# Kernel optimization log

Hardware: AMD Instinct MI355X
Metric: run time of the kernel (lower is better)

The kernel has to match this reference:

```python
import jax, jax.numpy as jnp
import numpy as np

# ---- cfg constants (JDE / YOLOv4-tracking style) ----
STRIDES = (8.0, 16.0, 32.0)
TRAIN_SIZE = 608.0
LEVELS = 3
NUM_ANCHORS = 4
EMB_DIM = 208
CONF_THRESH = 0.5
NMS_IOU = 0.45
K_LEVEL = 300   # proposals kept per level after confidence filtering
MAX_PROP = 500  # final padded proposal count per image
_ANCHORS = np.array([
    [[8, 24], [11, 34], [16, 48], [23, 68]],
    [[32, 96], [45, 135], [64, 192], [90, 271]],
    [[128, 384], [180, 540], [256, 640], [512, 640]],
], dtype=np.float32)  # [LEVELS, NUM_ANCHORS, 2] in pixels


def _decode_level(pred, emb, anchors_px, stride):
    """pred [B,A,H,W,6], emb [B,H,W,E] -> [B, A*H*W, 4+1+E] (xyxy in [0,1], conf, l2-norm emb)."""
    B, A, H, W, _ = pred.shape
    conf = jax.nn.softmax(pred[..., 4:6], axis=-1)[..., 1:2]  # [B,A,H,W,1]
    anc = anchors_px / stride  # anchors in grid units, [A,2]
    gy, gx = jnp.meshgrid(jnp.arange(H, dtype=pred.dtype),
                          jnp.arange(W, dtype=pred.dtype), indexing="ij")
    aw = anc[:, 0][:, None, None]  # [A,1,1]
    ah = anc[:, 1][:, None, None]
    # JDE-style delta decode: offsets scaled by anchor size, exp size decode
    x = pred[..., 0] * aw + gx
    y = pred[..., 1] * ah + gy
    w = jnp.exp(pred[..., 2]) * aw
    h = jnp.exp(pred[..., 3]) * ah
    scale = stride / TRAIN_SIZE  # back to pixels, then normalize by train size
    x1 = jnp.clip((x - 0.5 * w) * scale, 0.0, 1.0)
    y1 = jnp.clip((y - 0.5 * h) * scale, 0.0, 1.0)
    x2 = jnp.clip((x + 0.5 * w) * scale, 0.0, 1.0)
    y2 = jnp.clip((y + 0.5 * h) * scale, 0.0, 1.0)
    box = jnp.stack([x1, y1, x2, y2], axis=-1)  # [B,A,H,W,4]
    # tile embedding over anchors and l2-normalize (tf.math.l2_normalize, eps on sum of squares)
    pe = jnp.broadcast_to(emb[:, None], (B, A, H, W, emb.shape[-1]))
    n2 = jnp.sum(pe * pe, axis=-1, keepdims=True)
    pe = pe * jax.lax.rsqrt(jnp.maximum(n2, 1e-12))
    preds = jnp.concatenate([box, conf, pe], axis=-1)  # [B,A,H,W,4+1+E]
    return preds.reshape(B, A * H * W, preds.shape[-1])


def _conf_topk(props):
    """Confidence threshold + keep top K_LEVEL per image (zero-padded). props [B,N,D]."""
    s = props[..., 4]
    sm = jnp.where(s > CONF_THRESH, s, 0.0)
    top_s, top_i = jax.lax.top_k(sm, K_LEVEL)
    g = jnp.take_along_axis(props, top_i[..., None], axis=1)  # [B,K,D]
    return g * (top_s > 0.0)[..., None].astype(props.dtype)


def _nms_one(props):
    """Greedy NMS for one image. props [N,D] -> [MAX_PROP,D] zero-padded."""
    sc_in = props[:, 4]
    order = jnp.argsort(-sc_in)
    p = props[order]                      # sorted by score desc
    b, sc = p[:, :4], p[:, 4]
    N = b.shape[0]
    area = (b[:, 2] - b[:, 0]) * (b[:, 3] - b[:, 1])
    ix1 = jnp.maximum(b[:, None, 0], b[None, :, 0])
    iy1 = jnp.maximum(b[:, None, 1], b[None, :, 1])
    ix2 = jnp.minimum(b[:, None, 2], b[None, :, 2])
    iy2 = jnp.minimum(b[:, None, 3], b[None, :, 3])
    inter = jnp.clip(ix2 - ix1, 0.0) * jnp.clip(iy2 - iy1, 0.0)
    iou = inter / (area[:, None] + area[None, :] - inter + 1e-9)  # [N,N]
    idxs = jnp.arange(N)
    keep0 = sc > 0.0
    def step(keep, i):
        row = jnp.take(iou, i, axis=0)
        ki = jnp.take(keep, i)
        sup = ki & (row > NMS_IOU) & (idxs > i)
        return keep & jnp.logical_not(sup), None
    keep, _ = jax.lax.scan(step, keep0, idxs)
    keep = keep & (sc > 0.0)
    rank = jnp.cumsum(keep) - 1
    dest = jnp.where(keep & (rank < MAX_PROP), rank, MAX_PROP)  # out-of-range -> dropped
    out = jnp.zeros((MAX_PROP, p.shape[1]), p.dtype).at[dest].set(p, mode="drop")
    return out


def _forward(pred0, pred1, pred2, emb0, emb1, emb2):
    preds = (pred0, pred1, pred2)
    embs = (emb0, emb1, emb2)
    levels = []
    for i in range(LEVELS):
        pr = _decode_level(preds[i], embs[i], jnp.asarray(_ANCHORS[i]), STRIDES[i])
        levels.append(_conf_topk(pr))
    props = jnp.concatenate(levels, axis=1)        # [B, 3*K_LEVEL, 4+1+E]
    out = jax.vmap(_nms_one)(props)                # [B, MAX_PROP, 4+1+E]
    # entry_stop_gradients: grads only through non-zero (valid) entries
    mask = (jnp.sum(out[..., :4], axis=-1) != 0.0).astype(out.dtype)[..., None]
    return out * mask + jax.lax.stop_gradient(out) * (1.0 - mask)


def setup_inputs() -> dict:
    key = jax.random.key(0)
    ks = jax.random.split(key, 6)
    B = 16
    sizes = [76, 38, 19]  # TRAIN_SIZE // stride
    d = {}
    for i, hw in enumerate(sizes):
        d[f"pred{i}"] = jax.random.normal(ks[i], (B, NUM_ANCHORS, hw, hw, 6), jnp.float32)
        d[f"emb{i}"] = jax.random.normal(ks[3 + i], (B, hw, hw, EMB_DIM), jnp.float32)
    return d


def reference(pred0, pred1, pred2, emb0, emb1, emb2):
    return _forward(pred0, pred1, pred2, emb0, emb1, emb2)
```

## Files before the change

kernel.cpp:

```cpp
#include <hip/hip_runtime.h>

typedef unsigned long long u64;
typedef unsigned int u32;

#define KLVL 300
#define NPROP 900
#define MAXPROP 500
#define DDIM 213
#define EDIM 208

__constant__ float c_anc[3][4][2] = {
  {{1.0f, 3.0f}, {1.375f, 4.25f}, {2.0f, 6.0f}, {2.875f, 8.5f}},
  {{2.0f, 6.0f}, {2.8125f, 8.4375f}, {4.0f, 12.0f}, {5.625f, 16.9375f}},
  {{4.0f, 12.0f}, {5.625f, 16.875f}, {8.0f, 20.0f}, {16.0f, 20.0f}},
};
__constant__ float c_scale[3] = { (float)(8.0 / 608.0), (float)(16.0 / 608.0), (float)(32.0 / 608.0) };

__device__ __forceinline__ int level_H(int lvl) { return (lvl == 0) ? 76 : ((lvl == 1) ? 38 : 19); }

#define SB_STRIDE 30336
#define MASKT_STRIDE 904
#define MASK_IMG (15*904)
#define BOX_STRIDE 928
#define BOX_IMG (6*928)

#define OFF_SCORES 0
#define OFF_HIST   1945600
#define OFF_BUFTS  1945600
#define OFF_BUFTI  2142208
#define OFF_BUFGS  2338816
#define OFF_BUFGI  2437120
#define OFF_CNTG   2535424
#define OFF_CNTT   2535680
#define OFF_THR    2535936
#define OFF_CNT    2536192
#define OFF_SELS   2536448
#define OFF_SELI   2594048
#define OFF_BOX    2651904
#define OFF_SRC    3008256

__device__ __forceinline__ u64 readlane_u64(u64 v, int l) {
  u32 lo = (u32)__builtin_amdgcn_readlane((int)(u32)(v & 0xFFFFFFFFull), l);
  u32 hi = (u32)__builtin_amdgcn_readlane((int)(u32)(v >> 32), l);
  return ((u64)hi << 32) | (u64)lo;
}

__global__ __launch_bounds__(256) void score_kernel(
    const float* __restrict__ pred0, const float* __restrict__ pred1, const float* __restrict__ pred2,
    float* __restrict__ ws_scores, u32* __restrict__ hist)
{
  const int blk = blockIdx.x;
  const int b = blk / 120;
  const int r = blk % 120;
  int lvl, rb, N, off;
  const float* pred;
  if (r < 91)       { lvl = 0; rb = r;       N = 23104; off = 0;     pred = pred0; }
  else if (r < 114) { lvl = 1; rb = r - 91;  N = 5776;  off = 23104; pred = pred1; }
  else              { lvl = 2; rb = r - 114; N = 1444;  off = 28880; pred = pred2; }
  const int n = rb * 256 + (int)threadIdx.x;
  if (n >= N) return;
  const float* pb = pred + (size_t)b * N * 6;
  float2 l = *reinterpret_cast<const float2*>(pb + (size_t)n * 6 + 4);
  float m = fmaxf(l.x, l.y);
  float e0 = expf(l.x - m), e1 = expf(l.y - m);
  float s = e1 / (e0 + e1);
  float sm = (s > 0.5f) ? s : 0.0f;
  ws_scores[(size_t)b * SB_STRIDE + off + n] = sm;
  if (sm > 0.0f) {
    u32 key = __float_as_uint(sm) - 0x3F000000u;
    u32 bk = min(key >> 12, 2047u);
    atomicAdd(&hist[(u32)(b * 3 + lvl) * 2048u + bk], 1u);
  }
}

__global__ __launch_bounds__(256) void thresh_kernel(
    const u32* __restrict__ hist, int* __restrict__ thrT, int* __restrict__ cnt,
    u32* __restrict__ cntG, u32* __restrict__ cntT)
{
  __shared__ u32 wt[4];
  __shared__ int sT;
  const int bl = blockIdx.x, t = threadIdx.x, lane = t & 63, wid = t >> 6;
  const u32* h = hist + (size_t)bl * 2048;
  u32 hv[8]; u32 part = 0;
  #pragma unroll
  for (int q = 0; q < 8; ++q) { hv[q] = h[2047 - 8 * t - q]; part += hv[q]; }
  u32 incl = part;
  #pragma unroll
  for (int off = 1; off < 64; off <<= 1) { u32 v = __shfl_up(incl, (unsigned)off, 64); if (lane >= off) incl += v; }
  if (lane == 63) wt[wid] = incl;
  __syncthreads();
  u32 above = 0;
  for (int w2 = 0; w2 < wid; ++w2) above += wt[w2];
  const u32 total = wt[0] + wt[1] + wt[2] + wt[3];
  if (total > 300u) {
    u32 run = above + incl - part;
    #pragma unroll
    for (int q = 0; q < 8; ++q) {
      u32 hq = hv[q];
      if (hq && run < 300u && 300u <= run + hq) sT = 2047 - 8 * t - q;
      run += hq;
    }
  }
  __syncthreads();
  if (t == 0) {
    thrT[bl] = (total <= 300u) ? -1 : sT;
    cnt[bl] = (int)min(total, 300u);
    cntG[bl] = 0u; cntT[bl] = 0u;
  }
}

__global__ __launch_bounds__(256) void collect_kernel(
    const float* __restrict__ ws_scores, const int* __restrict__ thrT,
    u32* __restrict__ cntG, u32* __restrict__ cntT,
    float* __restrict__ bufGs, int* __restrict__ bufGi,
    float* __restrict__ bufTs, int* __restrict__ bufTi)
{
  const int blk = blockIdx.x;
  const int b = blk / 120;
  const int r = blk % 120;
  int lvl, rb, N, off;
  if (r < 91)       { lvl = 0; rb = r;       N = 23104; off = 0;     }
  else if (r < 114) { lvl = 1; rb = r - 91;  N = 5776;  off = 23104; }
  else              { lvl = 2; rb = r - 114; N = 1444;  off = 28880; }
  const int n = rb * 256 + (int)threadIdx.x;
  if (n >= N) return;
  float s = ws_scores[(size_t)b * SB_STRIDE + off + n];
  if (s <= 0.0f) return;
  u32 key = __float_as_uint(s) - 0x3F000000u;
  int bk = (int)min(key >> 12, 2047u);
  const int bl = b * 3 + lvl;
  const int T = thrT[bl];
  if (bk > T) {
    u32 p = atomicAdd(&cntG[bl], 1u);
    if (p < 512u) { bufGs[bl * 512 + p] = s; bufGi[bl * 512 + p] = n; }
  } else if (bk == T) {
    u32 p = atomicAdd(&cntT[bl], 1u);
    if (p < 1024u) { bufTs[bl * 1024 + p] = s; bufTi[bl * 1024 + p] = n; }
  }
}

__global__ __launch_bounds__(1024) void sort_kernel(
    const float* __restrict__ bufGs, const int* __restrict__ bufGi,
    const float* __restrict__ bufTs, const int* __restrict__ bufTi,
    const u32* __restrict__ cntG, const u32* __restrict__ cntT, const int* __restrict__ cnt,
    float* __restrict__ sel_score, int* __restrict__ sel_idx)
{
  __shared__ float gs[512]; __shared__ int gi[512];
  __shared__ float ts[1024]; __shared__ int ti[1024];
  const int bl = blockIdx.x, t = threadIdx.x;
  const int b = bl / 3, lvl = bl % 3;
  const int G = (int)min(cntG[bl], 512u);
  const int Tn = (int)min(cntT[bl], 1024u);
  const int selCnt = cnt[bl];
  if (t < G) { gs[t] = bufGs[bl * 512 + t]; gi[t] = bufGi[bl * 512 + t]; }
  if (t < Tn) { ts[t] = bufTs[bl * 1024 + t]; ti[t] = bufTi[bl * 1024 + t]; }
  __syncthreads();
  float* out_s = sel_score + (size_t)b * NPROP + (size_t)lvl * KLVL;
  int* out_i = sel_idx + (size_t)b * NPROP + (size_t)lvl * KLVL;
  if (t < G) {
    float sv = gs[t]; int iv = gi[t];
    int rk = 0;
    for (int j = 0; j < G; ++j) { float sj = gs[j]; int ij = gi[j]; rk += ((sj > sv) || (sj == sv && ij < iv)) ? 1 : 0; }
    out_s[rk] = sv; out_i[rk] = iv;
  }
  if (t < Tn) {
    float sv = ts[t]; int iv = ti[t];
    int rk = 0;
    for (int j = 0; j < Tn; ++j) { float sj = ts[j]; int ij = ti[j]; rk += ((sj > sv) || (sj == sv && ij < iv)) ? 1 : 0; }
    if (rk < selCnt - G) { out_s[G + rk] = sv; out_i[G + rk] = iv; }
  }
  for (int s2 = selCnt + t; s2 < KLVL; s2 += 1024) { out_s[s2] = 0.0f; out_i[s2] = 0; }
}

__global__ __launch_bounds__(512) void rank_kernel(
    const float* __restrict__ pred0, const float* __restrict__ pred1, const float* __restrict__ pred2,
    const float* __restrict__ sel_score, const int* __restrict__ sel_idx, const int* __restrict__ cnt,
    float* __restrict__ ws_box)
{
  __shared__ float s_sc[NPROP];
  __shared__ int s_c[3];
  const int bl = blockIdx.x, t = threadIdx.x;
  const int b = bl / 3, lvl = bl % 3;
  if (t < 3) s_c[t] = cnt[b * 3 + t];
  for (int i = t; i < NPROP; i += 512) s_sc[i] = sel_score[(size_t)b * NPROP + i];
  __syncthreads();
  const int pos = t;
  if (pos < s_c[lvl]) {
    const int slot = lvl * KLVL + pos;
    float sv = s_sc[slot];
    u32 rank = (u32)pos;
    for (int ol = 0; ol < 3; ++ol) {
      if (ol == lvl) continue;
      int base = ol * KLVL, co = s_c[ol];
      int lo2 = 0, hi2 = co;
      if (ol < lvl) {
        while (lo2 < hi2) { int mid = (lo2 + hi2) >> 1; if (s_sc[base + mid] >= sv) lo2 = mid + 1; else hi2 = mid; }
      } else {
        while (lo2 < hi2) { int mid = (lo2 + hi2) >> 1; if (s_sc[base + mid] > sv) lo2 = mid + 1; else hi2 = mid; }
      }
      rank += (u32)lo2;
    }
    int n = sel_idx[(size_t)b * NPROP + slot];
    int Hl = level_H(lvl), HWl = Hl * Hl;
    int a = n / HWl, rem = n - a * HWl, gy = rem / Hl, gx = rem - gy * Hl;
    const float* pred = (lvl == 0) ? pred0 : ((lvl == 1) ? pred1 : pred2);
    const float* p = pred + ((size_t)b * 4 * HWl + (size_t)n) * 6;
    float p0 = p[0], p1 = p[1], p2 = p[2], p3 = p[3];
    float aw = c_anc[lvl][a][0], ah = c_anc[lvl][a][1];
    float x = p0 * aw + (float)gx;
    float y = p1 * ah + (float)gy;
    float wv = expf(p2) * aw;
    float hv = expf(p3) * ah;
    float sc = c_scale[lvl];
    float x1 = fminf(fmaxf((x - 0.5f * wv) * sc, 0.0f), 1.0f);
    float y1 = fminf(fmaxf((y - 0.5f * hv) * sc, 0.0f), 1.0f);
    float x2 = fminf(fmaxf((x + 0.5f * wv) * sc, 0.0f), 1.0f);
    float y2 = fminf(fmaxf((y + 0.5f * hv) * sc, 0.0f), 1.0f);
    float* Bx = ws_box + (size_t)b * BOX_IMG;
    Bx[rank] = x1;
    Bx[BOX_STRIDE + rank] = y1;
    Bx[2 * BOX_STRIDE + rank] = x2;
    Bx[3 * BOX_STRIDE + rank] = y2;
    Bx[4 * BOX_STRIDE + rank] = sv;
    ((int*)(Bx + 5 * BOX_STRIDE))[rank] = slot;
  }
}

__global__ __launch_bounds__(256) void mask_kernel(
    const float* __restrict__ ws_box, const int* __restrict__ cnt, u64* __restrict__ ws_mask)
{
  const int w = blockIdx.x, b = blockIdx.y, t = threadIdx.x;
  const float* B = ws_box + (size_t)b * BOX_IMG;
  const float* X1 = B, * Y1 = B + BOX_STRIDE, * X2 = B + 2 * BOX_STRIDE, * Y2 = B + 3 * BOX_STRIDE;
  const int Np = cnt[b * 3] + cnt[b * 3 + 1] + cnt[b * 3 + 2];
  __shared__ float jx1[64], jy1[64], jx2[64], jy2[64], jar[64];
  if (t < 64) {
    int j = w * 64 + t;
    if (j < Np) {
      float a1 = X1[j], b1 = Y1[j], a2 = X2[j], b2 = Y2[j];
      jx1[t] = a1; jy1[t] = b1; jx2[t] = a2; jy2[t] = b2;
      jar[t] = (a2 - a1) * (b2 - b1);
    }
  }
  __syncthreads();
  u64* mkT = ws_mask + (size_t)b * MASK_IMG + (size_t)w * MASKT_STRIDE;
  const int j0 = w << 6;
  const int jlim = min(64, Np - j0);
  for (int i = t; i < 904; i += 256) {
    u64 bits = 0;
    if (i < Np && jlim > 0 && j0 + 63 > i) {
      float xi1 = X1[i], yi1 = Y1[i], xi2 = X2[i], yi2 = Y2[i];
      float ai = (xi2 - xi1) * (yi2 - yi1);
      for (int jj = 0; jj < jlim; ++jj) {
        int j = j0 + jj;
        if (j > i) {
          float xx1 = fmaxf(xi1, jx1[jj]);
          float yy1 = fmaxf(yi1, jy1[jj]);
          float xx2 = fminf(xi2, jx2[jj]);
          float yy2 = fminf(yi2, jy2[jj]);
          float iw = fmaxf(xx2 - xx1, 0.0f);
          float ih = fmaxf(yy2 - yy1, 0.0f);
          float inter = iw * ih;
          float iou = inter / (ai + jar[jj] - inter + 1e-9f);
          if (iou > 0.45f) bits |= (1ull << jj);
        }
      }
    }
    mkT[i] = bits;
  }
}

__global__ __launch_bounds__(64) void scan_kernel(
    const u64* __restrict__ ws_mask, const int* __restrict__ cnt, int* __restrict__ ws_src)
{
  __shared__ u64 s_keep[16];
  __shared__ u32 s_pre[16];
  const int b = blockIdx.x;
  const int lane = (int)threadIdx.x;
  const int Np = cnt[b * 3] + cnt[b * 3 + 1] + cnt[b * 3 + 2];
  const u64* mkT = ws_mask + (size_t)b * MASK_IMG;

#define DECL_DIAG(c) u64 d##c = mkT[(size_t)(c) * MASKT_STRIDE + (c) * 64 + lane];
  DECL_DIAG(0) DECL_DIAG(1) DECL_DIAG(2) DECL_DIAG(3) DECL_DIAG(4)
  DECL_DIAG(5) DECL_DIAG(6) DECL_DIAG(7) DECL_DIAG(8) DECL_DIAG(9)
  DECL_DIAG(10) DECL_DIAG(11) DECL_DIAG(12) DECL_DIAG(13) DECL_DIAG(14)
#undef DECL_DIAG

  u64 remv = 0;
  u64 keepw = 0;

#define TILE(c, dvar) \
  if ((c) * 64 < Np) { \
    u64 rv = readlane_u64(remv, (c)); \
    int rem_ = Np - (c) * 64; \
    u64 valid_ = (rem_ >= 64) ? ~0ull : ((1ull << rem_) - 1ull); \
    u64 live = valid_ & ~rv; \
    u64 keep = 0; \
    while (live) { \
      int j_ = (int)__builtin_ctzll(live); \
      keep |= (1ull << j_); \
      u64 row_ = readlane_u64(dvar, j_); \
      live &= ~(row_ | (1ull << j_)); \
    } \
    if (lane == (c)) keepw = keep; \
    if (keep && lane > (c) && lane < 15) { \
      const u64* colw_ = mkT + (size_t)lane * MASKT_STRIDE + (c) * 64; \
      u64 acc_ = 0; \
      _Pragma("unroll") \
      for (int ch_ = 0; ch_ < 8; ++ch_) { \
        u64 r0_ = colw_[ch_ * 8 + 0], r1_ = colw_[ch_ * 8 + 1], r2_ = colw_[ch_ * 8 + 2], r3_ = colw_[ch_ * 8 + 3]; \
        u64 r4_ = colw_[ch_ * 8 + 4], r5_ = colw_[ch_ * 8 + 5], r6_ = colw_[ch_ * 8 + 6], r7_ = colw_[ch_ * 8 + 7]; \
        u32 kb_ = (u32)((keep >> (ch_ * 8)) & 0xFFull); \
        acc_ |= (kb_ & 1u ? r0_ : 0) | (kb_ & 2u ? r1_ : 0) | (kb_ & 4u ? r2_ : 0) | (kb_ & 8u ? r3_ : 0) \
              | (kb_ & 16u ? r4_ : 0) | (kb_ & 32u ? r5_ : 0) | (kb_ & 64u ? r6_ : 0) | (kb_ & 128u ? r7_ : 0); \
      } \
      remv |= acc_; \
    } \
  }

  TILE(0, d0) TILE(1, d1) TILE(2, d2) TILE(3, d3) TILE(4, d4)
  TILE(5, d5) TILE(6, d6) TILE(7, d7) TILE(8, d8) TILE(9, d9)
  TILE(10, d10) TILE(11, d11) TILE(12, d12) TILE(13, d13) TILE(14, d14)
#undef TILE

  u32 pc = (lane < 15) ? (u32)__popcll(keepw) : 0u;
  u32 incl = pc;
  #pragma unroll
  for (int off = 1; off < 64; off <<= 1) { u32 v = __shfl_up(incl, (unsigned)off, 64); if (lane >= off) incl += v; }
  if (lane < 16) { s_keep[lane] = (lane < 15) ? keepw : 0ull; s_pre[lane] = incl - pc; }
  __syncthreads();

  int* src = ws_src + b * MAXPROP;
  for (int r = lane; r < MAXPROP; r += 64) src[r] = -1;
  for (int i = lane; i < Np; i += 64) {
    u64 kw = s_keep[i >> 6];
    if ((kw >> (i & 63)) & 1ull) {
      u32 rank = s_pre[i >> 6] + (u32)__popcll(kw & ((1ull << (i & 63)) - 1ull));
      if (rank < MAXPROP) src[rank] = i;
    }
  }
}

__global__ __launch_bounds__(256) void out_kernel(
    const float* __restrict__ emb0, const float* __restrict__ emb1, const float* __restrict__ emb2,
    const float* __restrict__ ws_box, const int* __restrict__ ws_src, const int* __restrict__ sel_idx,
    float* __restrict__ out)
{
  const int blk = blockIdx.x;
  const int b = blk / 125;
  const int r = (blk % 125) * 4 + ((int)threadIdx.x >> 6);
  const int lane = (int)threadIdx.x & 63;
  float* orow = out + ((size_t)b * MAXPROP + r) * DDIM;
  const int i = ws_src[b * MAXPROP + r];
  if (i < 0) {
    for (int c = lane; c < DDIM; c += 64) orow[c] = 0.0f;
    return;
  }
  const float* B = ws_box + (size_t)b * BOX_IMG;
  float x1 = B[i], y1 = B[BOX_STRIDE + i], x2 = B[2 * BOX_STRIDE + i], y2 = B[3 * BOX_STRIDE + i];
  float score = B[4 * BOX_STRIDE + i];
  int slot = ((const int*)(B + 5 * BOX_STRIDE))[i];
  int n = sel_idx[(size_t)b * NPROP + slot];
  int lvl = slot / KLVL;
  int Hl = level_H(lvl), HWl = Hl * Hl;
  int a = n / HWl, rem = n - a * HWl, gy = rem / Hl, gx = rem - gy * Hl;
  (void)a;
  const float* emb = (lvl == 0) ? emb0 : ((lvl == 1) ? emb1 : emb2);
  const float* e = emb + ((size_t)(b * Hl + gy) * Hl + gx) * EDIM;
  float v0 = e[lane], v1 = e[lane + 64], v2 = e[lane + 128];
  float v3 = (lane < 16) ? e[lane + 192] : 0.0f;
  float ss = v0 * v0 + v1 * v1 + v2 * v2 + v3 * v3;
  for (int off = 32; off > 0; off >>= 1) ss += __shfl_xor(ss, off, 64);
  float rs = 1.0f / sqrtf(fmaxf(ss, 1e-12f));
  if (lane == 0) {
    orow[0] = x1; orow[1] = y1; orow[2] = x2; orow[3] = y2; orow[4] = score;
  }
  orow[5 + lane] = v0 * rs;
  orow[5 + 64 + lane] = v1 * rs;
  orow[5 + 128 + lane] = v2 * rs;
  if (lane < 16) orow[5 + 192 + lane] = v3 * rs;
}

extern "C" void kernel_launch(void* const* d_in, const int* in_sizes, int n_in,
                              void* d_out, int out_size, void* d_ws, size_t ws_size,
                              hipStream_t stream) {
  const float* pred[3] = {nullptr, nullptr, nullptr};
  const float* emb[3] = {nullptr, nullptr, nullptr};
  for (int i = 0; i < n_in; ++i) {
    const float* p = (const float*)d_in[i];
    switch (in_sizes[i]) {
      case 2217984:  pred[0] = p; break;
      case 554496:   pred[1] = p; break;
      case 138624:   pred[2] = p; break;
      case 19222528: emb[0] = p; break;
      case 4805632:  emb[1] = p; break;
      case 1201408:  emb[2] = p; break;
      default: break;
    }
  }
  char* ws = (char*)d_ws;
  float* ws_scores = (float*)(ws + OFF_SCORES);
  u64* ws_mask = (u64*)(ws + OFF_SCORES);
  u32* hist = (u32*)(ws + OFF_HIST);
  float* bufTs = (float*)(ws + OFF_BUFTS);
  int* bufTi = (int*)(ws + OFF_BUFTI);
  float* bufGs = (float*)(ws + OFF_BUFGS);
  int* bufGi = (int*)(ws + OFF_BUFGI);
  u32* cntG = (u32*)(ws + OFF_CNTG);
  u32* cntT = (u32*)(ws + OFF_CNTT);
  int* thrT = (int*)(ws + OFF_THR);
  int* cnt = (int*)(ws + OFF_CNT);
  float* sel_score = (float*)(ws + OFF_SELS);
  int* sel_idx = (int*)(ws + OFF_SELI);
  float* ws_box = (float*)(ws + OFF_BOX);
  int* ws_src = (int*)(ws + OFF_SRC);

  hipMemsetAsync(hist, 0, 48 * 2048 * sizeof(u32), stream);
  score_kernel<<<dim3(1920), dim3(256), 0, stream>>>(pred[0], pred[1], pred[2], ws_scores, hist);
  thresh_kernel<<<dim3(48), dim3(256), 0, stream>>>(hist, thrT, cnt, cntG, cntT);
  collect_kernel<<<dim3(1920), dim3(256), 0, stream>>>(ws_scores, thrT, cntG, cntT, bufGs, bufGi, bufTs, bufTi);
  sort_kernel<<<dim3(48), dim3(1024), 0, stream>>>(bufGs, bufGi, bufTs, bufTi, cntG, cntT, cnt, sel_score, sel_idx);
  rank_kernel<<<dim3(48), dim3(512), 0, stream>>>(pred[0], pred[1], pred[2], sel_score, sel_idx, cnt, ws_box);
  mask_kernel<<<dim3(15, 16), dim3(256), 0, stream>>>(ws_box, cnt, ws_mask);
  scan_kernel<<<dim3(16), dim3(64), 0, stream>>>(ws_mask, cnt, ws_src);
  out_kernel<<<dim3(2000), dim3(256), 0, stream>>>(emb[0], emb[1], emb[2], ws_box, ws_src, sel_idx, (float*)d_out);
}
```

Measured before the change: 295.8 us.

## Fuse all proposal stages into one cooperative persistent kernel with grid syncs

Replaces the memset and eight separate kernel launches with a single cooperative kernel. It steps through score, threshold, collect, sort+rank, mask, scan and output phases using grid-wide syncs. The sort and rank stages are merged per image so sorted scores stay in shared memory, which removes the sel_score round trip. The aim is to cut launch overhead and inter-kernel gaps. The cost is grid.sync barriers, a grid capped at an assumed 256 CUs times occupancy, and single-block serial phases (sort, scan) that idle the rest of the grid.

```diff
diff --git a/kernel.cpp b/kernel.cpp
--- a/kernel.cpp
+++ b/kernel.cpp
@@ -1,4 +1,7 @@
 #include <hip/hip_runtime.h>
+#include <hip/hip_cooperative_groups.h>
+
+namespace cg = cooperative_groups;
 
 typedef unsigned long long u64;
 typedef unsigned int u32;
@@ -19,6 +22,7 @@
 __device__ __forceinline__ int level_H(int lvl) { return (lvl == 0) ? 76 : ((lvl == 1) ? 38 : 19); }
 
 #define SB_STRIDE 30336
+#define SB_USED   30324
 #define MASKT_STRIDE 904
 #define MASK_IMG (15*904)
 #define BOX_STRIDE 928
@@ -34,7 +38,6 @@
 #define OFF_CNTT   2535680
 #define OFF_THR    2535936
 #define OFF_CNT    2536192
-#define OFF_SELS   2536448
 #define OFF_SELI   2594048
 #define OFF_BOX    2651904
 #define OFF_SRC    3008256
@@ -45,340 +48,344 @@
   return ((u64)hi << 32) | (u64)lo;
 }
 
-__global__ __launch_bounds__(256) void score_kernel(
+__device__ __forceinline__ bool decode_idx(int idx, int& b, int& lvl, int& n) {
+  b = idx / SB_STRIDE;
+  int off = idx - b * SB_STRIDE;
+  if (off >= SB_USED) return false;
+  if (off < 23104)      { lvl = 0; n = off; }
+  else if (off < 28880) { lvl = 1; n = off - 23104; }
+  else                  { lvl = 2; n = off - 28880; }
+  return true;
+}
+
+__global__ __launch_bounds__(256, 2) void proposal_mega_kernel(
     const float* __restrict__ pred0, const float* __restrict__ pred1, const float* __restrict__ pred2,
-    float* __restrict__ ws_scores, u32* __restrict__ hist)
+    const float* __restrict__ emb0, const float* __restrict__ emb1, const float* __restrict__ emb2,
+    char* __restrict__ ws, float* __restrict__ out)
 {
-  const int blk = blockIdx.x;
-  const int b = blk / 120;
-  const int r = blk % 120;
-  int lvl, rb, N, off;
-  const float* pred;
-  if (r < 91)       { lvl = 0; rb = r;       N = 23104; off = 0;     pred = pred0; }
-  else if (r < 114) { lvl = 1; rb = r - 91;  N = 5776;  off = 23104; pred = pred1; }
-  else              { lvl = 2; rb = r - 114; N = 1444;  off = 28880; pred = pred2; }
-  const int n = rb * 256 + (int)threadIdx.x;
-  if (n >= N) return;
-  const float* pb = pred + (size_t)b * N * 6;
-  float2 l = *reinterpret_cast<const float2*>(pb + (size_t)n * 6 + 4);
-  float m = fmaxf(l.x, l.y);
-  float e0 = expf(l.x - m), e1 = expf(l.y - m);
-  float s = e1 / (e0 + e1);
-  float sm = (s > 0.5f) ? s : 0.0f;
-  ws_scores[(size_t)b * SB_STRIDE + off + n] = sm;
-  if (sm > 0.0f) {
-    u32 key = __float_as_uint(sm) - 0x3F000000u;
-    u32 bk = min(key >> 12, 2047u);
-    atomicAdd(&hist[(u32)(b * 3 + lvl) * 2048u + bk], 1u);
-  }
-}
-
-__global__ __launch_bounds__(256) void thresh_kernel(
-    const u32* __restrict__ hist, int* __restrict__ thrT, int* __restrict__ cnt,
-    u32* __restrict__ cntG, u32* __restrict__ cntT)
-{
-  __shared__ u32 wt[4];
-  __shared__ int sT;
-  const int bl = blockIdx.x, t = threadIdx.x, lane = t & 63, wid = t >> 6;
-  const u32* h = hist + (size_t)bl * 2048;
-  u32 hv[8]; u32 part = 0;
-  #pragma unroll
-  for (int q = 0; q < 8; ++q) { hv[q] = h[2047 - 8 * t - q]; part += hv[q]; }
-  u32 incl = part;
-  #pragma unroll
-  for (int off = 1; off < 64; off <<= 1) { u32 v = __shfl_up(incl, (unsigned)off, 64); if (lane >= off) incl += v; }
-  if (lane == 63) wt[wid] = incl;
-  __syncthreads();
-  u32 above = 0;
-  for (int w2 = 0; w2 < wid; ++w2) above += wt[w2];
-  const u32 total = wt[0] + wt[1] + wt[2] + wt[3];
-  if (total > 300u) {
-    u32 run = above + incl - part;
+  cg::grid_group grid = cg::this_grid();
+  const int t = (int)threadIdx.x;
+  const int blk = (int)blockIdx.x;
+  const int nblk = (int)gridDim.x;
+  const int gtid = blk * 256 + t;
+  const int nthr = nblk * 256;
+  const int lane = t & 63, wid = t >> 6;
+
+  float* scores = (float*)(ws + OFF_SCORES);
+  u64* maskT    = (u64*)(ws + OFF_SCORES);
+  u32* hist     = (u32*)(ws + OFF_HIST);
+  float* bufTs  = (float*)(ws + OFF_BUFTS);
+  int* bufTi    = (int*)(ws + OFF_BUFTI);
+  float* bufGs  = (float*)(ws + OFF_BUFGS);
+  int* bufGi    = (int*)(ws + OFF_BUFGI);
+  u32* cntG     = (u32*)(ws + OFF_CNTG);
+  u32* cntT     = (u32*)(ws + OFF_CNTT);
+  int* thrT     = (int*)(ws + OFF_THR);
+  int* cnt      = (int*)(ws + OFF_CNT);
+  int* sel_idx  = (int*)(ws + OFF_SELI);
+  float* ws_box = (float*)(ws + OFF_BOX);
+  int* ws_src   = (int*)(ws + OFF_SRC);
+
+  __shared__ float sh_gs[512];  __shared__ int sh_gi[512];
+  __shared__ float sh_ts[1024]; __shared__ int sh_ti[1024];
+  __shared__ float sh_sc[NPROP]; __shared__ int sh_ix[NPROP];
+  __shared__ float sh_jx1[64], sh_jy1[64], sh_jx2[64], sh_jy2[64], sh_jar[64];
+  __shared__ u32 sh_wt[4];
+  __shared__ int sh_sT;
+
+  for (int i = gtid; i < 48 * 2048; i += nthr) hist[i] = 0u;
+  grid.sync();
+
+  for (int idx = gtid; idx < 16 * SB_STRIDE; idx += nthr) {
+    int b, lvl, n;
+    if (!decode_idx(idx, b, lvl, n)) continue;
+    const float* pred = (lvl == 0) ? pred0 : ((lvl == 1) ? pred1 : pred2);
+    const int N = (lvl == 0) ? 23104 : ((lvl == 1) ? 5776 : 1444);
+    const float* pb = pred + (size_t)b * N * 6;
+    float2 l = *reinterpret_cast<const float2*>(pb + (size_t)n * 6 + 4);
+    float m = fmaxf(l.x, l.y);
+    float e0 = expf(l.x - m), e1 = expf(l.y - m);
+    float s = e1 / (e0 + e1);
+    float sm = (s > 0.5f) ? s : 0.0f;
+    scores[idx] = sm;
+    if (sm > 0.0f) {
+      u32 key = __float_as_uint(sm) - 0x3F000000u;
+      u32 bk = min(key >> 12, 2047u);
+      atomicAdd(&hist[(u32)(b * 3 + lvl) * 2048u + bk], 1u);
+    }
+  }
+  grid.sync();
+
+  for (int u = blk; u < 48; u += nblk) {
+    const u32* h = hist + (size_t)u * 2048;
+    u32 hv[8]; u32 part = 0;
     #pragma unroll
-    for (int q = 0; q < 8; ++q) {
-      u32 hq = hv[q];
-      if (hq && run < 300u && 300u <= run + hq) sT = 2047 - 8 * t - q;
-      run += hq;
-    }
-  }
-  __syncthreads();
-  if (t == 0) {
-    thrT[bl] = (total <= 300u) ? -1 : sT;
-    cnt[bl] = (int)min(total, 300u);
-    cntG[bl] = 0u; cntT[bl] = 0u;
-  }
-}
-
-__global__ __launch_bounds__(256) void collect_kernel(
-    const float* __restrict__ ws_scores, const int* __restrict__ thrT,
-    u32* __restrict__ cntG, u32* __restrict__ cntT,
-    float* __restrict__ bufGs, int* __restrict__ bufGi,
-    float* __restrict__ bufTs, int* __restrict__ bufTi)
-{
-  const int blk = blockIdx.x;
-  const int b = blk / 120;
-  const int r = blk % 120;
-  int lvl, rb, N, off;
-  if (r < 91)       { lvl = 0; rb = r;       N = 23104; off = 0;     }
-  else if (r < 114) { lvl = 1; rb = r - 91;  N = 5776;  off = 23104; }
-  else              { lvl = 2; rb = r - 114; N = 1444;  off = 28880; }
-  const int n = rb * 256 + (int)threadIdx.x;
-  if (n >= N) return;
-  float s = ws_scores[(size_t)b * SB_STRIDE + off + n];
-  if (s <= 0.0f) return;
-  u32 key = __float_as_uint(s) - 0x3F000000u;
-  int bk = (int)min(key >> 12, 2047u);
-  const int bl = b * 3 + lvl;
-  const int T = thrT[bl];
-  if (bk > T) {
-    u32 p = atomicAdd(&cntG[bl], 1u);
-    if (p < 512u) { bufGs[bl * 512 + p] = s; bufGi[bl * 512 + p] = n; }
-  } else if (bk == T) {
-    u32 p = atomicAdd(&cntT[bl], 1u);
-    if (p < 1024u) { bufTs[bl * 1024 + p] = s; bufTi[bl * 1024 + p] = n; }
-  }
-}
-
-__global__ __launch_bounds__(1024) void sort_kernel(
-    const float* __restrict__ bufGs, const int* __restrict__ bufGi,
-    const float* __restrict__ bufTs, const int* __restrict__ bufTi,
-    const u32* __restrict__ cntG, const u32* __restrict__ cntT, const int* __restrict__ cnt,
-    float* __restrict__ sel_score, int* __restrict__ sel_idx)
-{
-  __shared__ float gs[512]; __shared__ int gi[512];
-  __shared__ float ts[1024]; __shared__ int ti[1024];
-  const int bl = blockIdx.x, t = threadIdx.x;
-  const int b = bl / 3, lvl = bl % 3;
-  const int G = (int)min(cntG[bl], 512u);
-  const int Tn = (int)min(cntT[bl], 1024u);
-  const int selCnt = cnt[bl];
-  if (t < G) { gs[t] = bufGs[bl * 512 + t]; gi[t] = bufGi[bl * 512 + t]; }
-  if (t < Tn) { ts[t] = bufTs[bl * 1024 + t]; ti[t] = bufTi[bl * 1024 + t]; }
-  __syncthreads();
-  float* out_s = sel_score + (size_t)b * NPROP + (size_t)lvl * KLVL;
-  int* out_i = sel_idx + (size_t)b * NPROP + (size_t)lvl * KLVL;
-  if (t < G) {
-    float sv = gs[t]; int iv = gi[t];
-    int rk = 0;
-    for (int j = 0; j < G; ++j) { float sj = gs[j]; int ij = gi[j]; rk += ((sj > sv) || (sj == sv && ij < iv)) ? 1 : 0; }
-    out_s[rk] = sv; out_i[rk] = iv;
-  }
-  if (t < Tn) {
-    float sv = ts[t]; int iv = ti[t];
-    int rk = 0;
-    for (int j = 0; j < Tn; ++j) { float sj = ts[j]; int ij = ti[j]; rk += ((sj > sv) || (sj == sv && ij < iv)) ? 1 : 0; }
-    if (rk < selCnt - G) { out_s[G + rk] = sv; out_i[G + rk] = iv; }
-  }
-  for (int s2 = selCnt + t; s2 < KLVL; s2 += 1024) { out_s[s2] = 0.0f; out_i[s2] = 0; }
-}
-
-__global__ __launch_bounds__(512) void rank_kernel(
-    const float* __restrict__ pred0, const float* __restrict__ pred1, const float* __restrict__ pred2,
-    const float* __restrict__ sel_score, const int* __restrict__ sel_idx, const int* __restrict__ cnt,
-    float* __restrict__ ws_box)
-{
-  __shared__ float s_sc[NPROP];
-  __shared__ int s_c[3];
-  const int bl = blockIdx.x, t = threadIdx.x;
-  const int b = bl / 3, lvl = bl % 3;
-  if (t < 3) s_c[t] = cnt[b * 3 + t];
-  for (int i = t; i < NPROP; i += 512) s_sc[i] = sel_score[(size_t)b * NPROP + i];
-  __syncthreads();
-  const int pos = t;
-  if (pos < s_c[lvl]) {
-    const int slot = lvl * KLVL + pos;
-    float sv = s_sc[slot];
-    u32 rank = (u32)pos;
-    for (int ol = 0; ol < 3; ++ol) {
-      if (ol == lvl) continue;
-      int base = ol * KLVL, co = s_c[ol];
-      int lo2 = 0, hi2 = co;
-      if (ol < lvl) {
-        while (lo2 < hi2) { int mid = (lo2 + hi2) >> 1; if (s_sc[base + mid] >= sv) lo2 = mid + 1; else hi2 = mid; }
-      } else {
-        while (lo2 < hi2) { int mid = (lo2 + hi2) >> 1; if (s_sc[base + mid] > sv) lo2 = mid + 1; else hi2 = mid; }
-      }
-      rank += (u32)lo2;
-    }
+    for (int q = 0; q < 8; ++q) { hv[q] = h[2047 - 8 * t - q]; part += hv[q]; }
+    u32 incl = part;
+    #pragma unroll
+    for (int off = 1; off < 64; off <<= 1) { u32 v = __shfl_up(incl, (unsigned)off, 64); if (lane >= off) incl += v; }
+    if (lane == 63) sh_wt[wid] = incl;
+    __syncthreads();
+    u32 above = 0;
+    for (int w2 = 0; w2 < wid; ++w2) above += sh_wt[w2];
+    const u32 total = sh_wt[0] + sh_wt[1] + sh_wt[2] + sh_wt[3];
+    if (total > 300u) {
+      u32 run = above + incl - part;
+      #pragma unroll
+      for (int q = 0; q < 8; ++q) {
+        u32 hq = hv[q];
+        if (hq && run < 300u && 300u <= run + hq) sh_sT = 2047 - 8 * t - q;
+        run += hq;
+      }
+    }
+    __syncthreads();
+    if (t == 0) {
+      thrT[u] = (total <= 300u) ? -1 : sh_sT;
+      cnt[u] = (int)min(total, 300u);
+      cntG[u] = 0u; cntT[u] = 0u;
+    }
+    __syncthreads();
+  }
+  grid.sync();
+
+  for (int idx = gtid; idx < 16 * SB_STRIDE; idx += nthr) {
+    int b, lvl, n;
+    if (!decode_idx(idx, b, lvl, n)) continue;
+    float s = scores[idx];
+    if (s <= 0.0f) continue;
+    u32 key = __float_as_uint(s) - 0x3F000000u;
+    int bk = (int)min(key >> 12, 2047u);
+    const int bl = b * 3 + lvl;
+    const int T = thrT[bl];
+    if (bk > T) {
+      u32 p = atomicAdd(&cntG[bl], 1u);
+      if (p < 512u) { bufGs[bl * 512 + p] = s; bufGi[bl * 512 + p] = n; }
+    } else if (bk == T) {
+      u32 p = atomicAdd(&cntT[bl], 1u);
+      if (p < 1024u) { bufTs[bl * 1024 + p] = s; bufTi[bl * 1024 + p] = n; }
+    }
+  }
+  grid.sync();
+
+  for (int u = blk; u < 16; u += nblk) {
+    const int b = u;
+    for (int lvl = 0; lvl < 3; ++lvl) {
+      const int bl = b * 3 + lvl;
+      const int G = (int)min(cntG[bl], 512u);
+      const int Tn = (int)min(cntT[bl], 1024u);
+      const int selCnt = cnt[bl];
+      for (int i = t; i < G; i += 256) { sh_gs[i] = bufGs[bl * 512 + i]; sh_gi[i] = bufGi[bl * 512 + i]; }
+      for (int i = t; i < Tn; i += 256) { sh_ts[i] = bufTs[bl * 1024 + i]; sh_ti[i] = bufTi[bl * 1024 + i]; }
+      __syncthreads();
+      for (int i = t; i < G; i += 256) {
+        float sv = sh_gs[i]; int iv = sh_gi[i];
+        int rk = 0;
+        for (int j = 0; j < G; ++j) { float sj = sh_gs[j]; int ij = sh_gi[j]; rk += ((sj > sv) || (sj == sv && ij < iv)) ? 1 : 0; }
+        sh_sc[lvl * KLVL + rk] = sv; sh_ix[lvl * KLVL + rk] = iv;
+      }
+      for (int i = t; i < Tn; i += 256) {
+        float sv = sh_ts[i]; int iv = sh_ti[i];
+        int rk = 0;
+        for (int j = 0; j < Tn; ++j) { float sj = sh_ts[j]; int ij = sh_ti[j]; rk += ((sj > sv) || (sj == sv && ij < iv)) ? 1 : 0; }
+        if (rk < selCnt - G) { sh_sc[lvl * KLVL + G + rk] = sv; sh_ix[lvl * KLVL + G + rk] = iv; }
+      }
+      for (int i = selCnt + t; i < KLVL; i += 256) { sh_sc[lvl * KLVL + i] = 0.0f; sh_ix[lvl * KLVL + i] = 0; }
+      __syncthreads();
+    }
+    for (int i = t; i < NPROP; i += 256) sel_idx[(size_t)b * NPROP + i] = sh_ix[i];
+    const int c0 = cnt[b * 3], c1 = cnt[b * 3 + 1], c2 = cnt[b * 3 + 2];
+    for (int slot = t; slot < NPROP; slot += 256) {
+      const int lvl = slot / KLVL, pos = slot - lvl * KLVL;
+      const int cl = (lvl == 0) ? c0 : ((lvl == 1) ? c1 : c2);
+      if (pos >= cl) continue;
+      float sv = sh_sc[slot];
+      u32 rank = (u32)pos;
+      for (int ol = 0; ol < 3; ++ol) {
+        if (ol == lvl) continue;
+        int base = ol * KLVL;
+        int co = (ol == 0) ? c0 : ((ol == 1) ? c1 : c2);
+        int lo2 = 0, hi2 = co;
+        if (ol < lvl) {
+          while (lo2 < hi2) { int mid = (lo2 + hi2) >> 1; if (sh_sc[base + mid] >= sv) lo2 = mid + 1; else hi2 = mid; }
+        } else {
+          while (lo2 < hi2) { int mid = (lo2 + hi2) >> 1; if (sh_sc[base + mid] > sv) lo2 = mid + 1; else hi2 = mid; }
+        }
+        rank += (u32)lo2;
+      }
+      int n = sh_ix[slot];
+      int Hl = level_H(lvl), HWl = Hl * Hl;
+      int a = n / HWl, rem = n - a * HWl, gy = rem / Hl, gx = rem - gy * Hl;
+      const float* pred = (lvl == 0) ? pred0 : ((lvl == 1) ? pred1 : pred2);
+      const float* p = pred + ((size_t)b * 4 * HWl + (size_t)n) * 6;
+      float p0 = p[0], p1 = p[1], p2 = p[2], p3 = p[3];
+      float aw = c_anc[lvl][a][0], ah = c_anc[lvl][a][1];
+      float x = p0 * aw + (float)gx;
+      float y = p1 * ah + (float)gy;
+      float wv = expf(p2) * aw;
+      float hv = expf(p3) * ah;
+      float sc = c_scale[lvl];
+      float x1 = fminf(fmaxf((x - 0.5f * wv) * sc, 0.0f), 1.0f);
+      float y1 = fminf(fmaxf((y - 0.5f * hv) * sc, 0.0f), 1.0f);
+      float x2 = fminf(fmaxf((x + 0.5f * wv) * sc, 0.0f), 1.0f);
+      float y2 = fminf(fmaxf((y + 0.5f * hv) * sc, 0.0f), 1.0f);
+      float* Bx = ws_box + (size_t)b * BOX_IMG;
+      Bx[rank] = x1;
+      Bx[BOX_STRIDE + rank] = y1;
+      Bx[2 * BOX_STRIDE + rank] = x2;
+      Bx[3 * BOX_STRIDE + rank] = y2;
+      Bx[4 * BOX_STRIDE + rank] = sv;
+      ((int*)(Bx + 5 * BOX_STRIDE))[rank] = slot;
+    }
+    __syncthreads();
+  }
+  grid.sync();
+
+  for (int u = blk; u < 240; u += nblk) {
+    const int w = u % 15, b = u / 15;
+    const float* B = ws_box + (size_t)b * BOX_IMG;
+    const float* X1 = B, * Y1 = B + BOX_STRIDE, * X2 = B + 2 * BOX_STRIDE, * Y2 = B + 3 * BOX_STRIDE;
+    const int Np = cnt[b * 3] + cnt[b * 3 + 1] + cnt[b * 3 + 2];
+    if (t < 64) {
+      int j = w * 64 + t;
+      if (j < Np) {
+        float a1 = X1[j], b1 = Y1[j], a2 = X2[j], b2 = Y2[j];
+        sh_jx1[t] = a1; sh_jy1[t] = b1; sh_jx2[t] = a2; sh_jy2[t] = b2;
+        sh_jar[t] = (a2 - a1) * (b2 - b1);
+      }
+    }
+    __syncthreads();
+    u64* mk = maskT + (size_t)b * MASK_IMG + (size_t)w * MASKT_STRIDE;
+    const int j0 = w << 6;
+    const int jlim = min(64, Np - j0);
+    for (int i = t; i < MASKT_STRIDE; i += 256) {
+      u64 bits = 0;
+      if (i < Np && jlim > 0 && j0 + 63 > i) {
+        float xi1 = X1[i], yi1 = Y1[i], xi2 = X2[i], yi2 = Y2[i];
+        float ai = (xi2 - xi1) * (yi2 - yi1);
+        for (int jj = 0; jj < jlim; ++jj) {
+          int j = j0 + jj;
+          if (j > i) {
+            float xx1 = fmaxf(xi1, sh_jx1[jj]);
+            float yy1 = fmaxf(yi1, sh_jy1[jj]);
+            float xx2 = fminf(xi2, sh_jx2[jj]);
+            float yy2 = fminf(yi2, sh_jy2[jj]);
+            float iw = fmaxf(xx2 - xx1, 0.0f);
+            float ih = fmaxf(yy2 - yy1, 0.0f);
+            float inter = iw * ih;
+            float iou = inter / (ai + sh_jar[jj] - inter + 1e-9f);
+            if (iou > 0.45f) bits |= (1ull << jj);
+          }
+        }
+      }
+      mk[i] = bits;
+    }
+    __syncthreads();
+  }
+  grid.sync();
+
+  for (int u = blk; u < 16; u += nblk) {
+    if (t < 64) {
+      const int b = u;
+      const int Np = cnt[b * 3] + cnt[b * 3 + 1] + cnt[b * 3 + 2];
+      const u64* mkT = maskT + (size_t)b * MASK_IMG;
+
+#define DECL_DIAG(c) u64 d##c = mkT[(size_t)(c) * MASKT_STRIDE + (c) * 64 + lane];
+      DECL_DIAG(0) DECL_DIAG(1) DECL_DIAG(2) DECL_DIAG(3) DECL_DIAG(4)
+      DECL_DIAG(5) DECL_DIAG(6) DECL_DIAG(7) DECL_DIAG(8) DECL_DIAG(9)
+      DECL_DIAG(10) DECL_DIAG(11) DECL_DIAG(12) DECL_DIAG(13) DECL_DIAG(14)
+#undef DECL_DIAG
+
+      u64 remv = 0, keepw = 0;
+      u32 tot = 0;
+      const bool ldok = (lane < 15);
+
+#define TILE(c, dvar) \
+      if ((c) * 64 < Np && tot < (u32)MAXPROP) { \
+        u64 cw[64]; \
+        { \
+          const u64* colw_ = mkT + (size_t)lane * MASKT_STRIDE + (c) * 64; \
+          const bool ld_ = ldok && (lane > (c)); \
+          _Pragma("unroll") \
+          for (int k = 0; k < 64; ++k) cw[k] = ld_ ? colw_[k] : 0ull; \
+        } \
+        u64 rv = readlane_u64(remv, (c)); \
+        int rem_ = Np - (c) * 64; \
+        u64 valid_ = (rem_ >= 64) ? ~0ull : ((1ull << rem_) - 1ull); \
+        u64 live = valid_ & ~rv; \
+        u64 keep = 0; \
+        while (live) { \
+          int j_ = (int)__builtin_ctzll(live); \
+          keep |= (1ull << j_); \
+          u64 row_ = readlane_u64(dvar, j_); \
+          live &= ~(row_ | (1ull << j_)); \
+        } \
+        if (lane == (c)) keepw = keep; \
+        u64 acc_ = 0; \
+        _Pragma("unroll") \
+        for (int k = 0; k < 64; ++k) acc_ |= ((keep >> k) & 1ull) ? cw[k] : 0ull; \
+        remv |= acc_; \
+        tot += (u32)__popcll(keep); \
+      }
+
+      TILE(0, d0) TILE(1, d1) TILE(2, d2) TILE(3, d3) TILE(4, d4)
+      TILE(5, d5) TILE(6, d6) TILE(7, d7) TILE(8, d8) TILE(9, d9)
+      TILE(10, d10) TILE(11, d11) TILE(12, d12) TILE(13, d13) TILE(14, d14)
+#undef TILE
+
+      u32 pc = (lane < 15) ? (u32)__popcll(keepw) : 0u;
+      u32 incl = pc;
+      #pragma unroll
+      for (int off = 1; off < 64; off <<= 1) { u32 v = __shfl_up(incl, (unsigned)off, 64); if (lane >= off) incl += v; }
+      u32 excl = incl - pc;
+      int* src = ws_src + b * MAXPROP;
+      for (int r = lane; r < MAXPROP; r += 64) src[r] = -1;
+      for (int i = lane; i < Np; i += 64) {
+        int w = i >> 6;
+        u64 kw = readlane_u64(keepw, w);
+        u32 pre = (u32)__builtin_amdgcn_readlane((int)excl, w);
+        if ((kw >> (i & 63)) & 1ull) {
+          u32 rank = pre + (u32)__popcll(kw & ((1ull << (i & 63)) - 1ull));
+          if (rank < MAXPROP) src[rank] = i;
+        }
+      }
+    }
+    __syncthreads();
+  }
+  grid.sync();
+
+  for (int task = blk * 4 + wid; task < 16 * MAXPROP; task += nblk * 4) {
+    const int b = task / MAXPROP;
+    const int r = task - b * MAXPROP;
+    float* orow = out + ((size_t)b * MAXPROP + r) * DDIM;
+    const int i = ws_src[b * MAXPROP + r];
+    if (i < 0) {
+      for (int c = lane; c < DDIM; c += 64) orow[c] = 0.0f;
+      continue;
+    }
+    const float* B = ws_box + (size_t)b * BOX_IMG;
+    float x1 = B[i], y1 = B[BOX_STRIDE + i], x2 = B[2 * BOX_STRIDE + i], y2 = B[3 * BOX_STRIDE + i];
+    float score = B[4 * BOX_STRIDE + i];
+    int slot = ((const int*)(B + 5 * BOX_STRIDE))[i];
     int n = sel_idx[(size_t)b * NPROP + slot];
+    int lvl = slot / KLVL;
     int Hl = level_H(lvl), HWl = Hl * Hl;
     int a = n / HWl, rem = n - a * HWl, gy = rem / Hl, gx = rem - gy * Hl;
-    const float* pred = (lvl == 0) ? pred0 : ((lvl == 1) ? pred1 : pred2);
-    const float* p = pred + ((size_t)b * 4 * HWl + (size_t)n) * 6;
-    float p0 = p[0], p1 = p[1], p2 = p[2], p3 = p[3];
-    float aw = c_anc[lvl][a][0], ah = c_anc[lvl][a][1];
-    float x = p0 * aw + (float)gx;
-    float y = p1 * ah + (float)gy;
-    float wv = expf(p2) * aw;
-    float hv = expf(p3) * ah;
-    float sc = c_scale[lvl];
-    float x1 = fminf(fmaxf((x - 0.5f * wv) * sc, 0.0f), 1.0f);
-    float y1 = fminf(fmaxf((y - 0.5f * hv) * sc, 0.0f), 1.0f);
-    float x2 = fminf(fmaxf((x + 0.5f * wv) * sc, 0.0f), 1.0f);
-    float y2 = fminf(fmaxf((y + 0.5f * hv) * sc, 0.0f), 1.0f);
-    float* Bx = ws_box + (size_t)b * BOX_IMG;
-    Bx[rank] = x1;
-    Bx[BOX_STRIDE + rank] = y1;
-    Bx[2 * BOX_STRIDE + rank] = x2;
-    Bx[3 * BOX_STRIDE + rank] = y2;
-    Bx[4 * BOX_STRIDE + rank] = sv;
-    ((int*)(Bx + 5 * BOX_STRIDE))[rank] = slot;
-  }
-}
-
-__global__ __launch_bounds__(256) void mask_kernel(
-    const float* __restrict__ ws_box, const int* __restrict__ cnt, u64* __restrict__ ws_mask)
-{
-  const int w = blockIdx.x, b = blockIdx.y, t = threadIdx.x;
-  const float* B = ws_box + (size_t)b * BOX_IMG;
-  const float* X1 = B, * Y1 = B + BOX_STRIDE, * X2 = B + 2 * BOX_STRIDE, * Y2 = B + 3 * BOX_STRIDE;
-  const int Np = cnt[b * 3] + cnt[b * 3 + 1] + cnt[b * 3 + 2];
-  __shared__ float jx1[64], jy1[64], jx2[64], jy2[64], jar[64];
-  if (t < 64) {
-    int j = w * 64 + t;
-    if (j < Np) {
-      float a1 = X1[j], b1 = Y1[j], a2 = X2[j], b2 = Y2[j];
-      jx1[t] = a1; jy1[t] = b1; jx2[t] = a2; jy2[t] = b2;
-      jar[t] = (a2 - a1) * (b2 - b1);
-    }
-  }
-  __syncthreads();
-  u64* mkT = ws_mask + (size_t)b * MASK_IMG + (size_t)w * MASKT_STRIDE;
-  const int j0 = w << 6;
-  const int jlim = min(64, Np - j0);
-  for (int i = t; i < 904; i += 256) {
-    u64 bits = 0;
-    if (i < Np && jlim > 0 && j0 + 63 > i) {
-      float xi1 = X1[i], yi1 = Y1[i], xi2 = X2[i], yi2 = Y2[i];
-      float ai = (xi2 - xi1) * (yi2 - yi1);
-      for (int jj = 0; jj < jlim; ++jj) {
-        int j = j0 + jj;
-        if (j > i) {
-          float xx1 = fmaxf(xi1, jx1[jj]);
-          float yy1 = fmaxf(yi1, jy1[jj]);
-          float xx2 = fminf(xi2, jx2[jj]);
-          float yy2 = fminf(yi2, jy2[jj]);
-          float iw = fmaxf(xx2 - xx1, 0.0f);
-          float ih = fmaxf(yy2 - yy1, 0.0f);
-          float inter = iw * ih;
-          float iou = inter / (ai + jar[jj] - inter + 1e-9f);
-          if (iou > 0.45f) bits |= (1ull << jj);
-        }
-      }
-    }
-    mkT[i] = bits;
-  }
-}
-
-__global__ __launch_bounds__(64) void scan_kernel(
-    const u64* __restrict__ ws_mask, const int* __restrict__ cnt, int* __restrict__ ws_src)
-{
-  __shared__ u64 s_keep[16];
-  __shared__ u32 s_pre[16];
-  const int b = blockIdx.x;
-  const int lane = (int)threadIdx.x;
-  const int Np = cnt[b * 3] + cnt[b * 3 + 1] + cnt[b * 3 + 2];
-  const u64* mkT = ws_mask + (size_t)b * MASK_IMG;
-
-#define DECL_DIAG(c) u64 d##c = mkT[(size_t)(c) * MASKT_STRIDE + (c) * 64 + lane];
-  DECL_DIAG(0) DECL_DIAG(1) DECL_DIAG(2) DECL_DIAG(3) DECL_DIAG(4)
-  DECL_DIAG(5) DECL_DIAG(6) DECL_DIAG(7) DECL_DIAG(8) DECL_DIAG(9)
-  DECL_DIAG(10) DECL_DIAG(11) DECL_DIAG(12) DECL_DIAG(13) DECL_DIAG(14)
-#undef DECL_DIAG
-
-  u64 remv = 0;
-  u64 keepw = 0;
-
-#define TILE(c, dvar) \
-  if ((c) * 64 < Np) { \
-    u64 rv = readlane_u64(remv, (c)); \
-    int rem_ = Np - (c) * 64; \
-    u64 valid_ = (rem_ >= 64) ? ~0ull : ((1ull << rem_) - 1ull); \
-    u64 live = valid_ & ~rv; \
-    u64 keep = 0; \
-    while (live) { \
-      int j_ = (int)__builtin_ctzll(live); \
-      keep |= (1ull << j_); \
-      u64 row_ = readlane_u64(dvar, j_); \
-      live &= ~(row_ | (1ull << j_)); \
-    } \
-    if (lane == (c)) keepw = keep; \
-    if (keep && lane > (c) && lane < 15) { \
-      const u64* colw_ = mkT + (size_t)lane * MASKT_STRIDE + (c) * 64; \
-      u64 acc_ = 0; \
-      _Pragma("unroll") \
-      for (int ch_ = 0; ch_ < 8; ++ch_) { \
-        u64 r0_ = colw_[ch_ * 8 + 0], r1_ = colw_[ch_ * 8 + 1], r2_ = colw_[ch_ * 8 + 2], r3_ = colw_[ch_ * 8 + 3]; \
-        u64 r4_ = colw_[ch_ * 8 + 4], r5_ = colw_[ch_ * 8 + 5], r6_ = colw_[ch_ * 8 + 6], r7_ = colw_[ch_ * 8 + 7]; \
-        u32 kb_ = (u32)((keep >> (ch_ * 8)) & 0xFFull); \
-        acc_ |= (kb_ & 1u ? r0_ : 0) | (kb_ & 2u ? r1_ : 0) | (kb_ & 4u ? r2_ : 0) | (kb_ & 8u ? r3_ : 0) \
-              | (kb_ & 16u ? r4_ : 0) | (kb_ & 32u ? r5_ : 0) | (kb_ & 64u ? r6_ : 0) | (kb_ & 128u ? r7_ : 0); \
-      } \
-      remv |= acc_; \
-    } \
-  }
-
-  TILE(0, d0) TILE(1, d1) TILE(2, d2) TILE(3, d3) TILE(4, d4)
-  TILE(5, d5) TILE(6, d6) TILE(7, d7) TILE(8, d8) TILE(9, d9)
-  TILE(10, d10) TILE(11, d11) TILE(12, d12) TILE(13, d13) TILE(14, d14)
-#undef TILE
-
-  u32 pc = (lane < 15) ? (u32)__popcll(keepw) : 0u;
-  u32 incl = pc;
-  #pragma unroll
-  for (int off = 1; off < 64; off <<= 1) { u32 v = __shfl_up(incl, (unsigned)off, 64); if (lane >= off) incl += v; }
-  if (lane < 16) { s_keep[lane] = (lane < 15) ? keepw : 0ull; s_pre[lane] = incl - pc; }
-  __syncthreads();
-
-  int* src = ws_src + b * MAXPROP;
-  for (int r = lane; r < MAXPROP; r += 64) src[r] = -1;
-  for (int i = lane; i < Np; i += 64) {
-    u64 kw = s_keep[i >> 6];
-    if ((kw >> (i & 63)) & 1ull) {
-      u32 rank = s_pre[i >> 6] + (u32)__popcll(kw & ((1ull << (i & 63)) - 1ull));
-      if (rank < MAXPROP) src[rank] = i;
-    }
-  }
-}
-
-__global__ __launch_bounds__(256) void out_kernel(
-    const float* __restrict__ emb0, const float* __restrict__ emb1, const float* __restrict__ emb2,
-    const float* __restrict__ ws_box, const int* __restrict__ ws_src, const int* __restrict__ sel_idx,
-    float* __restrict__ out)
-{
-  const int blk = blockIdx.x;
-  const int b = blk / 125;
-  const int r = (blk % 125) * 4 + ((int)threadIdx.x >> 6);
-  const int lane = (int)threadIdx.x & 63;
-  float* orow = out + ((size_t)b * MAXPROP + r) * DDIM;
-  const int i = ws_src[b * MAXPROP + r];
-  if (i < 0) {
-    for (int c = lane; c < DDIM; c += 64) orow[c] = 0.0f;
-    return;
-  }
-  const float* B = ws_box + (size_t)b * BOX_IMG;
-  float x1 = B[i], y1 = B[BOX_STRIDE + i], x2 = B[2 * BOX_STRIDE + i], y2 = B[3 * BOX_STRIDE + i];
-  float score = B[4 * BOX_STRIDE + i];
-  int slot = ((const int*)(B + 5 * BOX_STRIDE))[i];
-  int n = sel_idx[(size_t)b * NPROP + slot];
-  int lvl = slot / KLVL;
-  int Hl = level_H(lvl), HWl = Hl * Hl;
-  int a = n / HWl, rem = n - a * HWl, gy = rem / Hl, gx = rem - gy * Hl;
-  (void)a;
-  const float* emb = (lvl == 0) ? emb0 : ((lvl == 1) ? emb1 : emb2);
-  const float* e = emb + ((size_t)(b * Hl + gy) * Hl + gx) * EDIM;
-  float v0 = e[lane], v1 = e[lane + 64], v2 = e[lane + 128];
-  float v3 = (lane < 16) ? e[lane + 192] : 0.0f;
-  float ss = v0 * v0 + v1 * v1 + v2 * v2 + v3 * v3;
-  for (int off = 32; off > 0; off >>= 1) ss += __shfl_xor(ss, off, 64);
-  float rs = 1.0f / sqrtf(fmaxf(ss, 1e-12f));
-  if (lane == 0) {
-    orow[0] = x1; orow[1] = y1; orow[2] = x2; orow[3] = y2; orow[4] = score;
-  }
-  orow[5 + lane] = v0 * rs;
-  orow[5 + 64 + lane] = v1 * rs;
-  orow[5 + 128 + lane] = v2 * rs;
-  if (lane < 16) orow[5 + 192 + lane] = v3 * rs;
+    (void)a;
+    const float* emb = (lvl == 0) ? emb0 : ((lvl == 1) ? emb1 : emb2);
+    const float* e = emb + ((size_t)(b * Hl + gy) * Hl + gx) * EDIM;
+    float v0 = e[lane], v1 = e[lane + 64], v2 = e[lane + 128];
+    float v3 = (lane < 16) ? e[lane + 192] : 0.0f;
+    float ss = v0 * v0 + v1 * v1 + v2 * v2 + v3 * v3;
+    for (int off = 32; off > 0; off >>= 1) ss += __shfl_xor(ss, off, 64);
+    float rs = 1.0f / sqrtf(fmaxf(ss, 1e-12f));
+    if (lane == 0) {
+      orow[0] = x1; orow[1] = y1; orow[2] = x2; orow[3] = y2; orow[4] = score;
+    }
+    orow[5 + lane] = v0 * rs;
+    orow[5 + 64 + lane] = v1 * rs;
+    orow[5 + 128 + lane] = v2 * rs;
+    if (lane < 16) orow[5 + 192 + lane] = v3 * rs;
+  }
 }
 
 extern "C" void kernel_launch(void* const* d_in, const int* in_sizes, int n_in,
@@ -398,30 +405,22 @@
       default: break;
     }
   }
-  char* ws = (char*)d_ws;
-  float* ws_scores = (float*)(ws + OFF_SCORES);
-  u64* ws_mask = (u64*)(ws + OFF_SCORES);
-  u32* hist = (u32*)(ws + OFF_HIST);
-  float* bufTs = (float*)(ws + OFF_BUFTS);
-  int* bufTi = (int*)(ws + OFF_BUFTI);
-  float* bufGs = (float*)(ws + OFF_BUFGS);
-  int* bufGi = (int*)(ws + OFF_BUFGI);
-  u32* cntG = (u32*)(ws + OFF_CNTG);
-  u32* cntT = (u32*)(ws + OFF_CNTT);
-  int* thrT = (int*)(ws + OFF_THR);
-  int* cnt = (int*)(ws + OFF_CNT);
-  float* sel_score = (float*)(ws + OFF_SELS);
-  int* sel_idx = (int*)(ws + OFF_SELI);
-  float* ws_box = (float*)(ws + OFF_BOX);
-  int* ws_src = (int*)(ws + OFF_SRC);
-
-  hipMemsetAsync(hist, 0, 48 * 2048 * sizeof(u32), stream);
-  score_kernel<<<dim3(1920), dim3(256), 0, stream>>>(pred[0], pred[1], pred[2], ws_scores, hist);
-  thresh_kernel<<<dim3(48), dim3(256), 0, stream>>>(hist, thrT, cnt, cntG, cntT);
-  collect_kernel<<<dim3(1920), dim3(256), 0, stream>>>(ws_scores, thrT, cntG, cntT, bufGs, bufGi, bufTs, bufTi);
-  sort_kernel<<<dim3(48), dim3(1024), 0, stream>>>(bufGs, bufGi, bufTs, bufTi, cntG, cntT, cnt, sel_score, sel_idx);
-  rank_kernel<<<dim3(48), dim3(512), 0, stream>>>(pred[0], pred[1], pred[2], sel_score, sel_idx, cnt, ws_box);
-  mask_kernel<<<dim3(15, 16), dim3(256), 0, stream>>>(ws_box, cnt, ws_mask);
-  scan_kernel<<<dim3(16), dim3(64), 0, stream>>>(ws_mask, cnt, ws_src);
-  out_kernel<<<dim3(2000), dim3(256), 0, stream>>>(emb[0], emb[1], emb[2], ws_box, ws_src, sel_idx, (float*)d_out);
+  const float* p0 = pred[0]; const float* p1 = pred[1]; const float* p2 = pred[2];
+  const float* e0 = emb[0];  const float* e1 = emb[1];  const float* e2 = emb[2];
+  char* wsp = (char*)d_ws;
+  float* op = (float*)d_out;
+
+  int grid = 512;
+  int nb = 0;
+  if (hipOccupancyMaxActiveBlocksPerMultiprocessor(&nb, (const void*)proposal_mega_kernel, 256, 0) == hipSuccess && nb > 0) {
+    int g = nb * 256;
+    if (g < grid) grid = g;
+  } else {
+    grid = 256;
+  }
+
+  void* args[] = {(void*)&p0, (void*)&p1, (void*)&p2, (void*)&e0, (void*)&e1, (void*)&e2,
+                  (void*)&wsp, (void*)&op};
+  hipLaunchCooperativeKernel((const void*)proposal_mega_kernel, dim3(grid), dim3(256),
+                             args, 0, stream);
 }
```

After: 596.0 us. 101% more time.
